# Kernel optimization log

Hardware: AMD Instinct MI355X
Metric: run time of the kernel (lower is better)

The kernel has to match this reference:

```python
import jax, jax.numpy as jnp
import numpy as np

SR = 16000
MAX_Q = 2.0
MIN_D, MAX_D = 0.1, 2.0
MIN_W = 2.0 * np.pi * 20.0 / SR  # 2*pi*20/sr, lowest cutoff in rad/sample
MIN_Q = 0.1
B, T = 32, 65536


def map_logspace(x, lo, hi):
    # log-spaced interpolation: x in [0,1] -> [lo, hi]
    return lo * (hi / lo) ** x


def segment_average(params, seg_ids, num_segments):
    # average params over each onset-delimited segment, broadcast back to [B,T,4]
    def one(p, s):
        sums = jax.ops.segment_sum(p, s, num_segments=num_segments)
        cnt = jax.ops.segment_sum(jnp.ones(s.shape, p.dtype), s, num_segments=num_segments)
        avg = sums / jnp.maximum(cnt, 1.0)[:, None]
        return avg[s]
    return jax.vmap(one)(params, seg_ids)


def pluck_comb(f0, mu, x):
    # Mathematically identical to the scatter-built dense (B,T,D) FIR in the
    # original: y[b,t] = x[b,t] - (1-alfa)*x[b, t-(z+1)] - alfa*x[b, t-(z+2)]
    # (lag k corresponds to coefficient slot k-1; out-of-range lags are zero).
    Tx = x.shape[1]
    p = f0 * mu                       # fractional pluck position in samples
    z = jnp.floor(p)
    alfa = p - z
    zi = z.astype(jnp.int32)
    t = jnp.arange(Tx, dtype=jnp.int32)[None, :]

    def lag(idx):
        g = jnp.take_along_axis(x, jnp.clip(idx, 0, Tx - 1), axis=1)
        return jnp.where(idx >= 0, g, jnp.zeros((), x.dtype))

    return x - (1.0 - alfa) * lag(t - (zi + 1)) - alfa * lag(t - (zi + 2))


def tv_lp_biquad(x, w_mod, q_mod):
    # Time-varying RBJ low-pass biquad, transposed direct-form II, coefficients
    # recomputed per sample from w_mod,q_mod in (0,1).
    w = map_logspace(w_mod, MIN_W, jnp.pi)     # cutoff rad/sample in [min_w, pi]
    q = map_logspace(q_mod, MIN_Q, MAX_Q)      # resonance in [0.1, max_q]
    cw, sw = jnp.cos(w), jnp.sin(w)
    alpha = sw / (2.0 * q)
    a0 = 1.0 + alpha
    b0 = (1.0 - cw) / (2.0 * a0)
    b1 = (1.0 - cw) / a0
    b2 = b0
    a1 = (-2.0 * cw) / a0
    a2 = (1.0 - alpha) / a0

    xs = tuple(jnp.swapaxes(a, 0, 1) for a in (x, b0, b1, b2, a1, a2))  # [T,B]

    def step(carry, inp):
        s1, s2 = carry
        xt, b0t, b1t, b2t, a1t, a2t = inp
        y = b0t * xt + s1
        s1n = b1t * xt - a1t * y + s2
        s2n = b2t * xt - a2t * y
        return (s1n, s2n), y

    Bx = x.shape[0]
    init = (jnp.zeros((Bx,), x.dtype), jnp.zeros((Bx,), x.dtype))
    _, y = jax.lax.scan(step, init, xs)
    return jnp.swapaxes(y, 0, 1)


def _forward(f0, x, params, onsets):
    Tx = x.shape[1]
    # segment ids: cumulative count of onsets along time
    seg_ids = jnp.cumsum(onsets.astype(jnp.int32), axis=1)
    params = segment_average(params, seg_ids, Tx + 1)
    distance = map_logspace(jax.nn.sigmoid(params[..., 0]), MIN_D, MAX_D)
    w_mod = jax.nn.sigmoid(params[..., 1])
    q_mod = jax.nn.sigmoid(params[..., 2])
    mu = jax.nn.sigmoid(params[..., 3])
    xd = x * distance
    xc = pluck_comb(f0, mu, xd)
    return tv_lp_biquad(xc, w_mod, q_mod)


def setup_inputs() -> dict:
    key = jax.random.key(0)
    k1, k2, k3, k4 = jax.random.split(key, 4)
    # f0 is a fundamental period in samples (80-160 Hz at sr=16k)
    f0 = 100.0 + 100.0 * jax.random.uniform(k1, (B, T), jnp.float32)
    x = jax.random.normal(k2, (B, T), jnp.float32)
    params = jax.random.normal(k3, (B, T, 4), jnp.float32)
    onsets = (jax.random.uniform(k4, (B, T)) < 1e-3).astype(jnp.int32)  # sparse note onsets
    return {"f0": f0, "input": x, "params": params, "onsets": onsets}


def reference(f0, input, params, onsets):
    return _forward(f0, input, params, onsets)
```

## Files before the change

kernel.cpp:

```cpp
#include <hip/hip_runtime.h>
#include <cstdint>


namespace {
constexpr int B = 32;
constexpr int T = 65536;
constexpr int MAXSEG = 2048;
constexpr int L = 16;
constexpr int NC = T / L;
constexpr int NCHT = B * NC;
constexpr int WV = 64;
constexpr int SPAN = T / WV;
constexpr int SB = 4096;
constexpr int HALO = 256;

constexpr float MIN_W_C  = 0.00785398163397448279f;
constexpr float LOG2_400 = 8.64385618977472436f;
constexpr float LOG2_20  = 4.32192809488736235f;

__device__ __forceinline__ float sigmoid_precise(float v) {
  return 1.0f / (1.0f + expf(-v));
}
__device__ __forceinline__ int pad16(int i) { return i + (i >> 4); }
}

__global__ void k_count(const int* __restrict__ onsets, int* __restrict__ cnt) {
  int gw = (blockIdx.x * blockDim.x + threadIdx.x) >> 6;
  int lane = threadIdx.x & 63;
  int b = gw / WV, wv = gw % WV;
  const int* po = onsets + b * T + wv * SPAN;
  int run = 0;
  for (int it = 0; it < SPAN / 64; ++it) {
    int o = po[it * 64 + lane];
    unsigned long long m = __ballot(o != 0);
    run += __popcll(m);
  }
  if (lane == 0) cnt[b * WV + wv] = run;
}

__global__ void k_scanbase(const int* __restrict__ cnt, int* __restrict__ basep,
                           int* __restrict__ nseg) {
  int b = threadIdx.x;
  if (b < B) {
    int run = 0;
    for (int c = 0; c < WV; ++c) { basep[b * WV + c] = run; run += cnt[b * WV + c]; }
    nseg[b] = run;
  }
}

__global__ void k_segids(const int* __restrict__ onsets, const int* __restrict__ basep,
                         unsigned short* __restrict__ seg_ids, int* __restrict__ onsetPos) {
  int gw = (blockIdx.x * blockDim.x + threadIdx.x) >> 6;
  int lane = threadIdx.x & 63;
  int b = gw / WV, wv = gw % WV;
  const int rb = b * T;
  int t0 = wv * SPAN;
  int run = basep[b * WV + wv];
  unsigned long long bm = (1ull << lane) - 1ull;
  for (int it = 0; it < SPAN / 64; ++it) {
    int t = t0 + it * 64 + lane;
    int o = onsets[rb + t] != 0;
    unsigned long long m = __ballot(o);
    int sid = run + __popcll(m & bm) + o;
    seg_ids[rb + t] = (unsigned short)min(sid, MAXSEG - 1);
    if (o && sid <= MAXSEG) onsetPos[b * MAXSEG + sid - 1] = t;
    run += __popcll(m);
  }
}

__global__ void k_segavg(const float* __restrict__ params, const int* __restrict__ onsetPos,
                         const int* __restrict__ nseg, float4* __restrict__ segc,
                         float* __restrict__ segd) {
  __shared__ float part[4][4];
  int b = blockIdx.x >> 6;
  int s0 = blockIdx.x & 63;
  int n = nseg[b];
  int tid = threadIdx.x;
  const float4* pp = (const float4*)params;
  for (int s = s0; s <= n; s += 64) {
    int start = (s == 0) ? 0 : onsetPos[b * MAXSEG + min(s, MAXSEG) - 1];
    int end   = (s == n) ? T : onsetPos[b * MAXSEG + min(s, MAXSEG - 1)];
    float a0 = 0.f, a1 = 0.f, a2 = 0.f, a3 = 0.f;
    for (int t = start + tid; t < end; t += 256) {
      float4 pv = pp[b * T + t];
      a0 += pv.x; a1 += pv.y; a2 += pv.z; a3 += pv.w;
    }
    for (int off = 32; off; off >>= 1) {
      a0 += __shfl_down(a0, off); a1 += __shfl_down(a1, off);
      a2 += __shfl_down(a2, off); a3 += __shfl_down(a3, off);
    }
    if ((tid & 63) == 0) {
      int w = tid >> 6;
      part[w][0] = a0; part[w][1] = a1; part[w][2] = a2; part[w][3] = a3;
    }
    __syncthreads();
    if (tid == 0) {
      float t0 = 0.f, t1 = 0.f, t2 = 0.f, t3 = 0.f;
      for (int w = 0; w < 4; ++w) {
        t0 += part[w][0]; t1 += part[w][1]; t2 += part[w][2]; t3 += part[w][3];
      }
      float inv = 1.0f / (float)max(end - start, 1);
      float av0 = t0 * inv, av1 = t1 * inv, av2 = t2 * inv, av3 = t3 * inv;
      float dist = 0.1f * exp2f(sigmoid_precise(av0) * LOG2_20);
      float wv   = MIN_W_C * exp2f(sigmoid_precise(av1) * LOG2_400);
      float qv   = 0.1f * exp2f(sigmoid_precise(av2) * LOG2_20);
      float mu   = sigmoid_precise(av3);
      float sw = sinf(wv), cw = cosf(wv);
      float alpha = sw / (2.0f * qv);
      float a0c = 1.0f + alpha;
      float b0 = (1.0f - cw) / (2.0f * a0c);
      float na1 = 2.0f * cw / a0c;
      float na2 = (alpha - 1.0f) / a0c;
      int sl = min(s, MAXSEG - 1);
      segc[b * MAXSEG + sl] = make_float4(mu, b0, na1, na2);
      segd[b * MAXSEG + sl] = dist;
    }
    __syncthreads();
  }
}

__device__ __forceinline__ void build_tile(int rb, int rs, int bs,
                                           const float* __restrict__ x,
                                           const unsigned short* __restrict__ seg,
                                           const float* __restrict__ segd,
                                           float* __restrict__ s_xd,
                                           int* __restrict__ s_sid) {
  int tid = threadIdx.x;
  for (int j = tid; j < SB + HALO; j += 256) {
    int tr = bs - HALO + j;
    float v = 0.f;
    if (tr >= 0) {
      int s = (int)seg[rb + tr];
      v = x[rb + tr] * segd[rs + s];
    }
    s_xd[pad16(j)] = v;
  }
  for (int j = tid; j < SB; j += 256) {
    s_sid[pad16(j)] = (int)seg[rb + bs + j];
  }
  __syncthreads();
}

__device__ __forceinline__ float comb_lds(int li, float ft, const float* __restrict__ s_xd,
                                          const int* __restrict__ s_sid, int rs,
                                          const float4* __restrict__ segc,
                                          float& na1, float& na2) {
  int s = s_sid[pad16(li)];
  float4 sc = segc[rs + s];
  float p = ft * sc.x;
  float z = floorf(p);
  float alfa = p - z;
  int zi = min((int)z, HALO - 8);
  int i1 = li - zi - 1 + HALO;
  float xl1 = s_xd[pad16(i1)];
  float xl2 = s_xd[pad16(i1 - 1)];
  float xc = s_xd[pad16(li + HALO)] - (1.f - alfa) * xl1 - alfa * xl2;
  na1 = sc.z; na2 = sc.w;
  return sc.y * xc;
}

__global__ void k_compose(const float* __restrict__ f0, const float* __restrict__ x,
                          const unsigned short* __restrict__ seg,
                          const float4* __restrict__ segc,
                          const float* __restrict__ segd, float* __restrict__ ctb) {
  __shared__ float s_xd[4624];
  __shared__ int s_sid[4352];
  int blk = blockIdx.x;
  int b = blk >> 4, part = blk & 15;
  int rb = b * T, rs = b * MAXSEG;
  int bs = part * SB;
  build_tile(rb, rs, bs, x, seg, segd, s_xd, s_sid);

  int tid = threadIdx.x;
  int t0l = tid * 16;
  int g = blk * 256 + tid;
  const float4* f4 = (const float4*)(f0 + rb + bs + t0l);
  float A00 = 1.f, A01 = 0.f, A10 = 0.f, A11 = 1.f, d0 = 0.f, d1 = 0.f;
#pragma unroll
  for (int k = 0; k < 4; ++k) {
    float4 fv = f4[k];
    float fs[4] = {fv.x, fv.y, fv.z, fv.w};
#pragma unroll
    for (int q = 0; q < 4; ++q) {
      int li = t0l + k * 4 + q;
      float na1, na2;
      float p0 = comb_lds(li, fs[q], s_xd, s_sid, rs, segc, na1, na2);
      float c0v = p0 * (2.f + na1);
      float c1v = p0 * (1.f + na2);
      float nA00 = fmaf(na1, A00, A10);
      float nA01 = fmaf(na1, A01, A11);
      float nd0  = fmaf(na1, d0, d1 + c0v);
      float nA10 = na2 * A00;
      float nA11 = na2 * A01;
      float nd1  = fmaf(na2, d0, c1v);
      A00 = nA00; A01 = nA01; A10 = nA10; A11 = nA11; d0 = nd0; d1 = nd1;
    }
  }
  ctb[0 * NCHT + g] = A00; ctb[1 * NCHT + g] = A01;
  ctb[2 * NCHT + g] = A10; ctb[3 * NCHT + g] = A11;
  ctb[4 * NCHT + g] = d0;  ctb[5 * NCHT + g] = d1;
}

__global__ void k_scanrows(const float* __restrict__ ctb, float* __restrict__ S1,
                           float* __restrict__ S2) {
  __shared__ float wagg[4][6];
  int b = blockIdx.x;
  int tid = threadIdx.x;
  int lane = tid & 63, w = tid >> 6;
  int base = b * NC + tid * 16;
  float A00 = 1.f, A01 = 0.f, A10 = 0.f, A11 = 1.f, d0 = 0.f, d1 = 0.f;
#pragma unroll
  for (int k = 0; k < 4; ++k) {
    float4 M00 = *(const float4*)(ctb + 0 * NCHT + base + k * 4);
    float4 M01 = *(const float4*)(ctb + 1 * NCHT + base + k * 4);
    float4 M10 = *(const float4*)(ctb + 2 * NCHT + base + k * 4);
    float4 M11 = *(const float4*)(ctb + 3 * NCHT + base + k * 4);
    float4 E0  = *(const float4*)(ctb + 4 * NCHT + base + k * 4);
    float4 E1  = *(const float4*)(ctb + 5 * NCHT + base + k * 4);
    float m00[4] = {M00.x, M00.y, M00.z, M00.w};
    float m01[4] = {M01.x, M01.y, M01.z, M01.w};
    float m10[4] = {M10.x, M10.y, M10.z, M10.w};
    float m11[4] = {M11.x, M11.y, M11.z, M11.w};
    float e0[4]  = {E0.x, E0.y, E0.z, E0.w};
    float e1[4]  = {E1.x, E1.y, E1.z, E1.w};
#pragma unroll
    for (int q = 0; q < 4; ++q) {
      float nA00 = fmaf(m00[q], A00, m01[q] * A10);
      float nA01 = fmaf(m00[q], A01, m01[q] * A11);
      float nA10 = fmaf(m10[q], A00, m11[q] * A10);
      float nA11 = fmaf(m10[q], A01, m11[q] * A11);
      float nd0  = fmaf(m00[q], d0, fmaf(m01[q], d1, e0[q]));
      float nd1  = fmaf(m10[q], d0, fmaf(m11[q], d1, e1[q]));
      A00 = nA00; A01 = nA01; A10 = nA10; A11 = nA11; d0 = nd0; d1 = nd1;
    }
  }
#pragma unroll
  for (int off = 1; off < 64; off <<= 1) {
    float P00 = __shfl_up(A00, off), P01 = __shfl_up(A01, off);
    float P10 = __shfl_up(A10, off), P11 = __shfl_up(A11, off);
    float Pd0 = __shfl_up(d0, off),  Pd1 = __shfl_up(d1, off);
    if (lane >= off) {
      float nA00 = fmaf(A00, P00, A01 * P10);
      float nA01 = fmaf(A00, P01, A01 * P11);
      float nA10 = fmaf(A10, P00, A11 * P10);
      float nA11 = fmaf(A10, P01, A11 * P11);
      float nd0  = fmaf(A00, Pd0, fmaf(A01, Pd1, d0));
      float nd1  = fmaf(A10, Pd0, fmaf(A11, Pd1, d1));
      A00 = nA00; A01 = nA01; A10 = nA10; A11 = nA11; d0 = nd0; d1 = nd1;
    }
  }
  if (lane == 63) {
    wagg[w][0] = A00; wagg[w][1] = A01; wagg[w][2] = A10;
    wagg[w][3] = A11; wagg[w][4] = d0;  wagg[w][5] = d1;
  }
  __syncthreads();
  float E00 = __shfl_up(A00, 1), E01 = __shfl_up(A01, 1);
  float E10 = __shfl_up(A10, 1), E11 = __shfl_up(A11, 1);
  float Ed0 = __shfl_up(d0, 1),  Ed1 = __shfl_up(d1, 1);
  if (lane == 0) { E00 = 1.f; E01 = 0.f; E10 = 0.f; E11 = 1.f; Ed0 = 0.f; Ed1 = 0.f; }
  float P00 = 1.f, P01 = 0.f, P10 = 0.f, P11 = 1.f, Pd0 = 0.f, Pd1 = 0.f;
  for (int i = 0; i < w; ++i) {
    float W00 = wagg[i][0], W01 = wagg[i][1], W10 = wagg[i][2];
    float W11 = wagg[i][3], Wd0 = wagg[i][4], Wd1 = wagg[i][5];
    float n00 = fmaf(W00, P00, W01 * P10);
    float n01 = fmaf(W00, P01, W01 * P11);
    float n10 = fmaf(W10, P00, W11 * P10);
    float n11 = fmaf(W10, P01, W11 * P11);
    float nd0 = fmaf(W00, Pd0, fmaf(W01, Pd1, Wd0));
    float nd1 = fmaf(W10, Pd0, fmaf(W11, Pd1, Wd1));
    P00 = n00; P01 = n01; P10 = n10; P11 = n11; Pd0 = nd0; Pd1 = nd1;
  }
  float s1 = fmaf(E00, Pd0, fmaf(E01, Pd1, Ed0));
  float s2 = fmaf(E10, Pd0, fmaf(E11, Pd1, Ed1));
#pragma unroll
  for (int k = 0; k < 4; ++k) {
    float4 M00 = *(const float4*)(ctb + 0 * NCHT + base + k * 4);
    float4 M01 = *(const float4*)(ctb + 1 * NCHT + base + k * 4);
    float4 M10 = *(const float4*)(ctb + 2 * NCHT + base + k * 4);
    float4 M11 = *(const float4*)(ctb + 3 * NCHT + base + k * 4);
    float4 E0  = *(const float4*)(ctb + 4 * NCHT + base + k * 4);
    float4 E1  = *(const float4*)(ctb + 5 * NCHT + base + k * 4);
    float m00[4] = {M00.x, M00.y, M00.z, M00.w};
    float m01[4] = {M01.x, M01.y, M01.z, M01.w};
    float m10[4] = {M10.x, M10.y, M10.z, M10.w};
    float m11[4] = {M11.x, M11.y, M11.z, M11.w};
    float e0[4]  = {E0.x, E0.y, E0.z, E0.w};
    float e1[4]  = {E1.x, E1.y, E1.z, E1.w};
    float o1[4], o2[4];
#pragma unroll
    for (int q = 0; q < 4; ++q) {
      o1[q] = s1; o2[q] = s2;
      float t1 = fmaf(m00[q], s1, fmaf(m01[q], s2, e0[q]));
      float t2 = fmaf(m10[q], s1, fmaf(m11[q], s2, e1[q]));
      s1 = t1; s2 = t2;
    }
    *(float4*)(S1 + base + k * 4) = make_float4(o1[0], o1[1], o1[2], o1[3]);
    *(float4*)(S2 + base + k * 4) = make_float4(o2[0], o2[1], o2[2], o2[3]);
  }
}

__global__ void k_apply(const float* __restrict__ f0, const float* __restrict__ x,
                        const unsigned short* __restrict__ seg,
                        const float4* __restrict__ segc,
                        const float* __restrict__ segd, const float* __restrict__ S1,
                        const float* __restrict__ S2, float* __restrict__ out) {
  __shared__ float s_xd[4624];
  __shared__ int s_sid[4352];
  int blk = blockIdx.x;
  int b = blk >> 4, part = blk & 15;
  int rb = b * T, rs = b * MAXSEG;
  int bs = part * SB;
  build_tile(rb, rs, bs, x, seg, segd, s_xd, s_sid);

  int tid = threadIdx.x;
  int t0l = tid * 16;
  int g = blk * 256 + tid;
  const float4* f4 = (const float4*)(f0 + rb + bs + t0l);
  float4* o4 = (float4*)(out + rb + bs + t0l);
  float s1 = S1[g], s2 = S2[g];
#pragma unroll
  for (int k = 0; k < 4; ++k) {
    float4 fv = f4[k];
    float fs[4] = {fv.x, fv.y, fv.z, fv.w};
    float ys[4];
#pragma unroll
    for (int q = 0; q < 4; ++q) {
      int li = t0l + k * 4 + q;
      float na1, na2;
      float p0 = comb_lds(li, fs[q], s_xd, s_sid, rs, segc, na1, na2);
      float y = p0 + s1;
      ys[q] = y;
      float ns1 = fmaf(na1, y, fmaf(2.f, p0, s2));
      float ns2 = fmaf(na2, y, p0);
      s1 = ns1; s2 = ns2;
    }
    o4[k] = make_float4(ys[0], ys[1], ys[2], ys[3]);
  }
}

extern "C" void kernel_launch(void* const* d_in, const int* in_sizes, int n_in,
                              void* d_out, int out_size, void* d_ws, size_t ws_size,
                              hipStream_t stream) {
  const float* f0     = (const float*)d_in[0];
  const float* x      = (const float*)d_in[1];
  const float* params = (const float*)d_in[2];
  const int*   onsets = (const int*)d_in[3];
  float* out = (float*)d_out;

  char* w = (char*)d_ws;
  auto alloc = [&](size_t bytes) -> void* {
    void* p = (void*)w;
    w += (bytes + 255) & ~(size_t)255;
    return p;
  };
  unsigned short* seg_ids = (unsigned short*)alloc(sizeof(unsigned short) * B * T);
  int*    cnt      = (int*)alloc(sizeof(int) * B * WV);
  int*    basep    = (int*)alloc(sizeof(int) * B * WV);
  int*    nseg     = (int*)alloc(sizeof(int) * B);
  int*    onsetPos = (int*)alloc(sizeof(int) * B * MAXSEG);
  float4* segc     = (float4*)alloc(sizeof(float4) * B * MAXSEG);
  float*  segd     = (float*)alloc(sizeof(float) * B * MAXSEG);
  float*  ctb      = (float*)alloc(sizeof(float) * 6 * NCHT);
  float*  S1       = (float*)alloc(sizeof(float) * NCHT);
  float*  S2       = (float*)alloc(sizeof(float) * NCHT);
  (void)in_sizes; (void)n_in; (void)out_size; (void)ws_size;

  k_count   <<<512, 256, 0, stream>>>(onsets, cnt);
  k_scanbase<<<1, 64, 0, stream>>>(cnt, basep, nseg);
  k_segids  <<<512, 256, 0, stream>>>(onsets, basep, seg_ids, onsetPos);
  k_segavg  <<<B * 64, 256, 0, stream>>>(params, onsetPos, nseg, segc, segd);
  k_compose <<<NCHT / 256, 256, 0, stream>>>(f0, x, seg_ids, segc, segd, ctb);
  k_scanrows<<<B, 256, 0, stream>>>(ctb, S1, S2);
  k_apply   <<<NCHT / 256, 256, 0, stream>>>(f0, x, seg_ids, segc, segd, S1, S2, out);
}
```

Before: 141.2 us.

## Fuse biquad compose, row scan and apply into one decoupled-lookback kernel

Merges the three-pass chunked linear-recurrence scan (compose, per-row scan, apply) into a single kernel. Blocks take ticket-ordered tile ids and chain tile prefixes across the row with decoupled lookback using atomic flags. Per-sample comb outputs and coefficients stay in registers between the compose and apply phases, so the shared-memory tile is built once and the ctb/S1/S2 global round trips go away. It also folds the scanbase kernel into warp reductions inside segids and segavg, and vectorises the onset count. The cost is serial spin-waiting across blocks and higher register pressure from the 16-element caches.

```diff
diff --git a/kernel.cpp b/kernel.cpp
--- a/kernel.cpp
+++ b/kernel.cpp
@@ -6,13 +6,12 @@
 constexpr int B = 32;
 constexpr int T = 65536;
 constexpr int MAXSEG = 2048;
-constexpr int L = 16;
-constexpr int NC = T / L;
-constexpr int NCHT = B * NC;
 constexpr int WV = 64;
 constexpr int SPAN = T / WV;
 constexpr int SB = 4096;
 constexpr int HALO = 256;
+constexpr int PARTS = T / SB;
+constexpr int NB = B * PARTS;
 
 constexpr float MIN_W_C  = 0.00785398163397448279f;
 constexpr float LOG2_400 = 8.64385618977472436f;
@@ -22,40 +21,69 @@
   return 1.0f / (1.0f + expf(-v));
 }
 __device__ __forceinline__ int pad16(int i) { return i + (i >> 4); }
-}
-
-__global__ void k_count(const int* __restrict__ onsets, int* __restrict__ cnt) {
+
+struct Xf { float m00, m01, m10, m11, d0, d1; };
+__device__ __forceinline__ Xf xf_comp(const Xf& l, const Xf& e) {
+  Xf r;
+  r.m00 = fmaf(l.m00, e.m00, l.m01 * e.m10);
+  r.m01 = fmaf(l.m00, e.m01, l.m01 * e.m11);
+  r.m10 = fmaf(l.m10, e.m00, l.m11 * e.m10);
+  r.m11 = fmaf(l.m10, e.m01, l.m11 * e.m11);
+  r.d0  = fmaf(l.m00, e.d0, fmaf(l.m01, e.d1, l.d0));
+  r.d1  = fmaf(l.m10, e.d0, fmaf(l.m11, e.d1, l.d1));
+  return r;
+}
+__device__ __forceinline__ void xf_store(float* p, const Xf& v) {
+  __hip_atomic_store(&p[0], v.m00, __ATOMIC_RELAXED, __HIP_MEMORY_SCOPE_AGENT);
+  __hip_atomic_store(&p[1], v.m01, __ATOMIC_RELAXED, __HIP_MEMORY_SCOPE_AGENT);
+  __hip_atomic_store(&p[2], v.m10, __ATOMIC_RELAXED, __HIP_MEMORY_SCOPE_AGENT);
+  __hip_atomic_store(&p[3], v.m11, __ATOMIC_RELAXED, __HIP_MEMORY_SCOPE_AGENT);
+  __hip_atomic_store(&p[4], v.d0,  __ATOMIC_RELAXED, __HIP_MEMORY_SCOPE_AGENT);
+  __hip_atomic_store(&p[5], v.d1,  __ATOMIC_RELAXED, __HIP_MEMORY_SCOPE_AGENT);
+}
+__device__ __forceinline__ Xf xf_load(const float* p) {
+  Xf v;
+  v.m00 = __hip_atomic_load(&p[0], __ATOMIC_RELAXED, __HIP_MEMORY_SCOPE_AGENT);
+  v.m01 = __hip_atomic_load(&p[1], __ATOMIC_RELAXED, __HIP_MEMORY_SCOPE_AGENT);
+  v.m10 = __hip_atomic_load(&p[2], __ATOMIC_RELAXED, __HIP_MEMORY_SCOPE_AGENT);
+  v.m11 = __hip_atomic_load(&p[3], __ATOMIC_RELAXED, __HIP_MEMORY_SCOPE_AGENT);
+  v.d0  = __hip_atomic_load(&p[4], __ATOMIC_RELAXED, __HIP_MEMORY_SCOPE_AGENT);
+  v.d1  = __hip_atomic_load(&p[5], __ATOMIC_RELAXED, __HIP_MEMORY_SCOPE_AGENT);
+  return v;
+}
+}
+
+__global__ void k_count(const int* __restrict__ onsets, int* __restrict__ cnt,
+                        int* __restrict__ aggF, int* __restrict__ prefF,
+                        int* __restrict__ ticket) {
+  if (threadIdx.x == 0) {
+    aggF[blockIdx.x] = 0;
+    prefF[blockIdx.x] = 0;
+    if (blockIdx.x == 0) *ticket = 0;
+  }
   int gw = (blockIdx.x * blockDim.x + threadIdx.x) >> 6;
   int lane = threadIdx.x & 63;
   int b = gw / WV, wv = gw % WV;
-  const int* po = onsets + b * T + wv * SPAN;
+  const int4* po = (const int4*)(onsets + b * T + wv * SPAN);
   int run = 0;
-  for (int it = 0; it < SPAN / 64; ++it) {
-    int o = po[it * 64 + lane];
-    unsigned long long m = __ballot(o != 0);
-    run += __popcll(m);
-  }
+  for (int it = 0; it < SPAN / 256; ++it) {
+    int4 v = po[it * 64 + lane];
+    run += (v.x != 0) + (v.y != 0) + (v.z != 0) + (v.w != 0);
+  }
+  for (int off = 32; off; off >>= 1) run += __shfl_down(run, off);
   if (lane == 0) cnt[b * WV + wv] = run;
 }
 
-__global__ void k_scanbase(const int* __restrict__ cnt, int* __restrict__ basep,
-                           int* __restrict__ nseg) {
-  int b = threadIdx.x;
-  if (b < B) {
-    int run = 0;
-    for (int c = 0; c < WV; ++c) { basep[b * WV + c] = run; run += cnt[b * WV + c]; }
-    nseg[b] = run;
-  }
-}
-
-__global__ void k_segids(const int* __restrict__ onsets, const int* __restrict__ basep,
+__global__ void k_segids(const int* __restrict__ onsets, const int* __restrict__ cnt,
                          unsigned short* __restrict__ seg_ids, int* __restrict__ onsetPos) {
   int gw = (blockIdx.x * blockDim.x + threadIdx.x) >> 6;
   int lane = threadIdx.x & 63;
   int b = gw / WV, wv = gw % WV;
   const int rb = b * T;
   int t0 = wv * SPAN;
-  int run = basep[b * WV + wv];
+  int cl = (lane < wv) ? cnt[b * WV + lane] : 0;
+  for (int off = 1; off < 64; off <<= 1) cl += __shfl_xor(cl, off);
+  int run = cl;
   unsigned long long bm = (1ull << lane) - 1ull;
   for (int it = 0; it < SPAN / 64; ++it) {
     int t = t0 + it * 64 + lane;
@@ -69,13 +97,20 @@
 }
 
 __global__ void k_segavg(const float* __restrict__ params, const int* __restrict__ onsetPos,
-                         const int* __restrict__ nseg, float4* __restrict__ segc,
+                         const int* __restrict__ cnt, float4* __restrict__ segc,
                          float* __restrict__ segd) {
   __shared__ float part[4][4];
+  __shared__ int s_n;
   int b = blockIdx.x >> 6;
   int s0 = blockIdx.x & 63;
-  int n = nseg[b];
   int tid = threadIdx.x;
+  if (tid < 64) {
+    int v = cnt[b * WV + tid];
+    for (int off = 32; off; off >>= 1) v += __shfl_down(v, off);
+    if (tid == 0) s_n = v;
+  }
+  __syncthreads();
+  int n = s_n;
   const float4* pp = (const float4*)params;
   for (int s = s0; s <= n; s += 64) {
     int start = (s == 0) ? 0 : onsetPos[b * MAXSEG + min(s, MAXSEG) - 1];
@@ -119,13 +154,25 @@
   }
 }
 
-__device__ __forceinline__ void build_tile(int rb, int rs, int bs,
-                                           const float* __restrict__ x,
-                                           const unsigned short* __restrict__ seg,
-                                           const float* __restrict__ segd,
-                                           float* __restrict__ s_xd,
-                                           int* __restrict__ s_sid) {
+__global__ void __launch_bounds__(256, 2) k_fused(
+    const float* __restrict__ f0, const float* __restrict__ x,
+    const unsigned short* __restrict__ seg, const float4* __restrict__ segc,
+    const float* __restrict__ segd, float* __restrict__ out,
+    int* __restrict__ aggF, int* __restrict__ prefF,
+    float* __restrict__ aggP, float* __restrict__ prefP,
+    int* __restrict__ ticket) {
+  __shared__ float s_xd[4624];
+  __shared__ int s_sid[4352];
+  __shared__ float wagg[4][6];
+  __shared__ float rowpref[2];
+  __shared__ int s_tk;
   int tid = threadIdx.x;
+  if (tid == 0) s_tk = atomicAdd(ticket, 1);
+  __syncthreads();
+  int tk = s_tk;
+  int b = tk >> 4, part = tk & (PARTS - 1);
+  int rb = b * T, rs = b * MAXSEG, bs = part * SB;
+
   for (int j = tid; j < SB + HALO; j += 256) {
     int tr = bs - HALO + j;
     float v = 0.f;
@@ -135,46 +182,13 @@
     }
     s_xd[pad16(j)] = v;
   }
-  for (int j = tid; j < SB; j += 256) {
-    s_sid[pad16(j)] = (int)seg[rb + bs + j];
-  }
-  __syncthreads();
-}
-
-__device__ __forceinline__ float comb_lds(int li, float ft, const float* __restrict__ s_xd,
-                                          const int* __restrict__ s_sid, int rs,
-                                          const float4* __restrict__ segc,
-                                          float& na1, float& na2) {
-  int s = s_sid[pad16(li)];
-  float4 sc = segc[rs + s];
-  float p = ft * sc.x;
-  float z = floorf(p);
-  float alfa = p - z;
-  int zi = min((int)z, HALO - 8);
-  int i1 = li - zi - 1 + HALO;
-  float xl1 = s_xd[pad16(i1)];
-  float xl2 = s_xd[pad16(i1 - 1)];
-  float xc = s_xd[pad16(li + HALO)] - (1.f - alfa) * xl1 - alfa * xl2;
-  na1 = sc.z; na2 = sc.w;
-  return sc.y * xc;
-}
-
-__global__ void k_compose(const float* __restrict__ f0, const float* __restrict__ x,
-                          const unsigned short* __restrict__ seg,
-                          const float4* __restrict__ segc,
-                          const float* __restrict__ segd, float* __restrict__ ctb) {
-  __shared__ float s_xd[4624];
-  __shared__ int s_sid[4352];
-  int blk = blockIdx.x;
-  int b = blk >> 4, part = blk & 15;
-  int rb = b * T, rs = b * MAXSEG;
-  int bs = part * SB;
-  build_tile(rb, rs, bs, x, seg, segd, s_xd, s_sid);
-
-  int tid = threadIdx.x;
+  for (int j = tid; j < SB; j += 256) s_sid[pad16(j)] = (int)seg[rb + bs + j];
+  __syncthreads();
+
+  int lane = tid & 63, w = tid >> 6;
   int t0l = tid * 16;
-  int g = blk * 256 + tid;
   const float4* f4 = (const float4*)(f0 + rb + bs + t0l);
+  float p0c[16], na1c[16], na2c[16];
   float A00 = 1.f, A01 = 0.f, A10 = 0.f, A11 = 1.f, d0 = 0.f, d1 = 0.f;
 #pragma unroll
   for (int k = 0; k < 4; ++k) {
@@ -182,9 +196,21 @@
     float fs[4] = {fv.x, fv.y, fv.z, fv.w};
 #pragma unroll
     for (int q = 0; q < 4; ++q) {
-      int li = t0l + k * 4 + q;
-      float na1, na2;
-      float p0 = comb_lds(li, fs[q], s_xd, s_sid, rs, segc, na1, na2);
+      int idx = k * 4 + q;
+      int li = t0l + idx;
+      int s = s_sid[pad16(li)];
+      float4 sc = segc[rs + s];
+      float p = fs[q] * sc.x;
+      float z = floorf(p);
+      float alfa = p - z;
+      int zi = min((int)z, HALO - 8);
+      int i1 = li - zi - 1 + HALO;
+      float xl1 = s_xd[pad16(i1)];
+      float xl2 = s_xd[pad16(i1 - 1)];
+      float xc = s_xd[pad16(li + HALO)] - (1.f - alfa) * xl1 - alfa * xl2;
+      float p0 = sc.y * xc;
+      float na1 = sc.z, na2 = sc.w;
+      p0c[idx] = p0; na1c[idx] = na1; na2c[idx] = na2;
       float c0v = p0 * (2.f + na1);
       float c1v = p0 * (1.f + na2);
       float nA00 = fmaf(na1, A00, A10);
@@ -193,44 +219,6 @@
       float nA10 = na2 * A00;
       float nA11 = na2 * A01;
       float nd1  = fmaf(na2, d0, c1v);
-      A00 = nA00; A01 = nA01; A10 = nA10; A11 = nA11; d0 = nd0; d1 = nd1;
-    }
-  }
-  ctb[0 * NCHT + g] = A00; ctb[1 * NCHT + g] = A01;
-  ctb[2 * NCHT + g] = A10; ctb[3 * NCHT + g] = A11;
-  ctb[4 * NCHT + g] = d0;  ctb[5 * NCHT + g] = d1;
-}
-
-__global__ void k_scanrows(const float* __restrict__ ctb, float* __restrict__ S1,
-                           float* __restrict__ S2) {
-  __shared__ float wagg[4][6];
-  int b = blockIdx.x;
-  int tid = threadIdx.x;
-  int lane = tid & 63, w = tid >> 6;
-  int base = b * NC + tid * 16;
-  float A00 = 1.f, A01 = 0.f, A10 = 0.f, A11 = 1.f, d0 = 0.f, d1 = 0.f;
-#pragma unroll
-  for (int k = 0; k < 4; ++k) {
-    float4 M00 = *(const float4*)(ctb + 0 * NCHT + base + k * 4);
-    float4 M01 = *(const float4*)(ctb + 1 * NCHT + base + k * 4);
-    float4 M10 = *(const float4*)(ctb + 2 * NCHT + base + k * 4);
-    float4 M11 = *(const float4*)(ctb + 3 * NCHT + base + k * 4);
-    float4 E0  = *(const float4*)(ctb + 4 * NCHT + base + k * 4);
-    float4 E1  = *(const float4*)(ctb + 5 * NCHT + base + k * 4);
-    float m00[4] = {M00.x, M00.y, M00.z, M00.w};
-    float m01[4] = {M01.x, M01.y, M01.z, M01.w};
-    float m10[4] = {M10.x, M10.y, M10.z, M10.w};
-    float m11[4] = {M11.x, M11.y, M11.z, M11.w};
-    float e0[4]  = {E0.x, E0.y, E0.z, E0.w};
-    float e1[4]  = {E1.x, E1.y, E1.z, E1.w};
-#pragma unroll
-    for (int q = 0; q < 4; ++q) {
-      float nA00 = fmaf(m00[q], A00, m01[q] * A10);
-      float nA01 = fmaf(m00[q], A01, m01[q] * A11);
-      float nA10 = fmaf(m10[q], A00, m11[q] * A10);
-      float nA11 = fmaf(m10[q], A01, m11[q] * A11);
-      float nd0  = fmaf(m00[q], d0, fmaf(m01[q], d1, e0[q]));
-      float nd1  = fmaf(m10[q], d0, fmaf(m11[q], d1, e1[q]));
       A00 = nA00; A01 = nA01; A10 = nA10; A11 = nA11; d0 = nd0; d1 = nd1;
     }
   }
@@ -270,68 +258,64 @@
     float nd1 = fmaf(W10, Pd0, fmaf(W11, Pd1, Wd1));
     P00 = n00; P01 = n01; P10 = n10; P11 = n11; Pd0 = nd0; Pd1 = nd1;
   }
-  float s1 = fmaf(E00, Pd0, fmaf(E01, Pd1, Ed0));
-  float s2 = fmaf(E10, Pd0, fmaf(E11, Pd1, Ed1));
+  float X00 = fmaf(E00, P00, E01 * P10);
+  float X01 = fmaf(E00, P01, E01 * P11);
+  float X10 = fmaf(E10, P00, E11 * P10);
+  float X11 = fmaf(E10, P01, E11 * P11);
+  float Xd0 = fmaf(E00, Pd0, fmaf(E01, Pd1, Ed0));
+  float Xd1 = fmaf(E10, Pd0, fmaf(E11, Pd1, Ed1));
+
+  if (tid == 0) {
+    Xf G = {wagg[0][0], wagg[0][1], wagg[0][2], wagg[0][3], wagg[0][4], wagg[0][5]};
+    for (int i = 1; i < 4; ++i) {
+      Xf Wi = {wagg[i][0], wagg[i][1], wagg[i][2], wagg[i][3], wagg[i][4], wagg[i][5]};
+      G = xf_comp(Wi, G);
+    }
+    if (part == 0) {
+      xf_store(prefP + tk * 6, G);
+      __hip_atomic_store(&prefF[tk], 1, __ATOMIC_RELEASE, __HIP_MEMORY_SCOPE_AGENT);
+      rowpref[0] = 0.f; rowpref[1] = 0.f;
+    } else {
+      xf_store(aggP + tk * 6, G);
+      __hip_atomic_store(&aggF[tk], 1, __ATOMIC_RELEASE, __HIP_MEMORY_SCOPE_AGENT);
+      Xf R = {1.f, 0.f, 0.f, 1.f, 0.f, 0.f};
+      for (int j = part - 1; j >= 0; --j) {
+        int sidx = tk - (part - j);
+        bool got_pref = false;
+        for (;;) {
+          if (__hip_atomic_load(&prefF[sidx], __ATOMIC_ACQUIRE, __HIP_MEMORY_SCOPE_AGENT)) {
+            R = xf_comp(R, xf_load(prefP + sidx * 6));
+            got_pref = true; break;
+          }
+          if (__hip_atomic_load(&aggF[sidx], __ATOMIC_ACQUIRE, __HIP_MEMORY_SCOPE_AGENT)) {
+            R = xf_comp(R, xf_load(aggP + sidx * 6));
+            break;
+          }
+          __builtin_amdgcn_s_sleep(1);
+        }
+        if (got_pref) break;
+      }
+      Xf I = xf_comp(G, R);
+      xf_store(prefP + tk * 6, I);
+      __hip_atomic_store(&prefF[tk], 1, __ATOMIC_RELEASE, __HIP_MEMORY_SCOPE_AGENT);
+      rowpref[0] = R.d0; rowpref[1] = R.d1;
+    }
+  }
+  __syncthreads();
+  float s1 = fmaf(X00, rowpref[0], fmaf(X01, rowpref[1], Xd0));
+  float s2 = fmaf(X10, rowpref[0], fmaf(X11, rowpref[1], Xd1));
+  float4* o4 = (float4*)(out + rb + bs + t0l);
 #pragma unroll
   for (int k = 0; k < 4; ++k) {
-    float4 M00 = *(const float4*)(ctb + 0 * NCHT + base + k * 4);
-    float4 M01 = *(const float4*)(ctb + 1 * NCHT + base + k * 4);
-    float4 M10 = *(const float4*)(ctb + 2 * NCHT + base + k * 4);
-    float4 M11 = *(const float4*)(ctb + 3 * NCHT + base + k * 4);
-    float4 E0  = *(const float4*)(ctb + 4 * NCHT + base + k * 4);
-    float4 E1  = *(const float4*)(ctb + 5 * NCHT + base + k * 4);
-    float m00[4] = {M00.x, M00.y, M00.z, M00.w};
-    float m01[4] = {M01.x, M01.y, M01.z, M01.w};
-    float m10[4] = {M10.x, M10.y, M10.z, M10.w};
-    float m11[4] = {M11.x, M11.y, M11.z, M11.w};
-    float e0[4]  = {E0.x, E0.y, E0.z, E0.w};
-    float e1[4]  = {E1.x, E1.y, E1.z, E1.w};
-    float o1[4], o2[4];
+    float ys[4];
 #pragma unroll
     for (int q = 0; q < 4; ++q) {
-      o1[q] = s1; o2[q] = s2;
-      float t1 = fmaf(m00[q], s1, fmaf(m01[q], s2, e0[q]));
-      float t2 = fmaf(m10[q], s1, fmaf(m11[q], s2, e1[q]));
-      s1 = t1; s2 = t2;
-    }
-    *(float4*)(S1 + base + k * 4) = make_float4(o1[0], o1[1], o1[2], o1[3]);
-    *(float4*)(S2 + base + k * 4) = make_float4(o2[0], o2[1], o2[2], o2[3]);
-  }
-}
-
-__global__ void k_apply(const float* __restrict__ f0, const float* __restrict__ x,
-                        const unsigned short* __restrict__ seg,
-                        const float4* __restrict__ segc,
-                        const float* __restrict__ segd, const float* __restrict__ S1,
-                        const float* __restrict__ S2, float* __restrict__ out) {
-  __shared__ float s_xd[4624];
-  __shared__ int s_sid[4352];
-  int blk = blockIdx.x;
-  int b = blk >> 4, part = blk & 15;
-  int rb = b * T, rs = b * MAXSEG;
-  int bs = part * SB;
-  build_tile(rb, rs, bs, x, seg, segd, s_xd, s_sid);
-
-  int tid = threadIdx.x;
-  int t0l = tid * 16;
-  int g = blk * 256 + tid;
-  const float4* f4 = (const float4*)(f0 + rb + bs + t0l);
-  float4* o4 = (float4*)(out + rb + bs + t0l);
-  float s1 = S1[g], s2 = S2[g];
-#pragma unroll
-  for (int k = 0; k < 4; ++k) {
-    float4 fv = f4[k];
-    float fs[4] = {fv.x, fv.y, fv.z, fv.w};
-    float ys[4];
-#pragma unroll
-    for (int q = 0; q < 4; ++q) {
-      int li = t0l + k * 4 + q;
-      float na1, na2;
-      float p0 = comb_lds(li, fs[q], s_xd, s_sid, rs, segc, na1, na2);
+      int idx = k * 4 + q;
+      float p0 = p0c[idx];
       float y = p0 + s1;
       ys[q] = y;
-      float ns1 = fmaf(na1, y, fmaf(2.f, p0, s2));
-      float ns2 = fmaf(na2, y, p0);
+      float ns1 = fmaf(na1c[idx], y, fmaf(2.f, p0, s2));
+      float ns2 = fmaf(na2c[idx], y, p0);
       s1 = ns1; s2 = ns2;
     }
     o4[k] = make_float4(ys[0], ys[1], ys[2], ys[3]);
@@ -355,21 +339,19 @@
   };
   unsigned short* seg_ids = (unsigned short*)alloc(sizeof(unsigned short) * B * T);
   int*    cnt      = (int*)alloc(sizeof(int) * B * WV);
-  int*    basep    = (int*)alloc(sizeof(int) * B * WV);
-  int*    nseg     = (int*)alloc(sizeof(int) * B);
   int*    onsetPos = (int*)alloc(sizeof(int) * B * MAXSEG);
   float4* segc     = (float4*)alloc(sizeof(float4) * B * MAXSEG);
   float*  segd     = (float*)alloc(sizeof(float) * B * MAXSEG);
-  float*  ctb      = (float*)alloc(sizeof(float) * 6 * NCHT);
-  float*  S1       = (float*)alloc(sizeof(float) * NCHT);
-  float*  S2       = (float*)alloc(sizeof(float) * NCHT);
+  int*    aggF     = (int*)alloc(sizeof(int) * NB);
+  int*    prefF    = (int*)alloc(sizeof(int) * NB);
+  float*  aggP     = (float*)alloc(sizeof(float) * 6 * NB);
+  float*  prefP    = (float*)alloc(sizeof(float) * 6 * NB);
+  int*    ticket   = (int*)alloc(sizeof(int));
   (void)in_sizes; (void)n_in; (void)out_size; (void)ws_size;
 
-  k_count   <<<512, 256, 0, stream>>>(onsets, cnt);
-  k_scanbase<<<1, 64, 0, stream>>>(cnt, basep, nseg);
-  k_segids  <<<512, 256, 0, stream>>>(onsets, basep, seg_ids, onsetPos);
-  k_segavg  <<<B * 64, 256, 0, stream>>>(params, onsetPos, nseg, segc, segd);
-  k_compose <<<NCHT / 256, 256, 0, stream>>>(f0, x, seg_ids, segc, segd, ctb);
-  k_scanrows<<<B, 256, 0, stream>>>(ctb, S1, S2);
-  k_apply   <<<NCHT / 256, 256, 0, stream>>>(f0, x, seg_ids, segc, segd, S1, S2, out);
-}
+  k_count <<<NB, 256, 0, stream>>>(onsets, cnt, aggF, prefF, ticket);
+  k_segids<<<NB, 256, 0, stream>>>(onsets, cnt, seg_ids, onsetPos);
+  k_segavg<<<B * 64, 256, 0, stream>>>(params, onsetPos, cnt, segc, segd);
+  k_fused <<<NB, 256, 0, stream>>>(f0, x, seg_ids, segc, segd, out,
+                                   aggF, prefF, aggP, prefP, ticket);
+}
```

After: 189.7 us. 1.34x slower.
